# Optimization experiments

Measured on AMD Instinct MI355X. Metric: run time of the kernel, lower is better.

The kernel has to match this reference:

```python
import jax, jax.numpy as jnp
import numpy as np

ALPHA = 0.25
GAMMA = 2.0
COST_MASK = 1.0
COST_DICE = 1.0


def setup_inputs() -> dict:
    key = jax.random.key(0)
    k1, k2 = jax.random.split(key)
    B, N, M, H, W = 4, 100, 20, 256, 256
    outputs = jax.random.normal(k1, (B, N, H, W), dtype=jnp.float32)
    # binary target masks; threshold ensures every mask is non-empty so the
    # data-dependent tgt_ids truncation in the original is a no-op
    targets = (jax.random.uniform(k2, (B, M, H, W)) > 0.7).astype(jnp.float32)
    return {"outputs": outputs, "targets": targets}


def _cost_matrix(out_mask, tgt_mask):
    # out_mask: [N, HW] logits, tgt_mask: [M, HW] binary
    hw = out_mask.shape[1]
    prob = jax.nn.sigmoid(out_mask)
    # BCE-with-logits: target=1 -> softplus(-x); target=0 -> softplus(x)
    bce_pos = jax.nn.softplus(-out_mask)
    bce_neg = jax.nn.softplus(out_mask)
    focal_pos = ALPHA * (1.0 - prob) ** GAMMA * bce_pos            # [N, HW]
    focal_neg = (1.0 - ALPHA) * prob ** GAMMA * bce_neg            # [N, HW]
    cost_mask = (jnp.einsum('nc,mc->nm', focal_pos, tgt_mask)
                 + jnp.einsum('nc,mc->nm', focal_neg, 1.0 - tgt_mask)) / hw
    # dice cost
    numerator = 2.0 * jnp.einsum('nc,mc->nm', prob, tgt_mask)
    denominator = prob.sum(-1)[:, None] + tgt_mask.sum(-1)[None, :]
    cost_dice = 1.0 - (numerator + 1.0) / (denominator + 1.0)
    return COST_MASK * cost_mask + COST_DICE * cost_dice           # [N, M]


def reference(outputs, targets):
    B, N, H, W = outputs.shape
    M = targets.shape[1]
    out_flat = outputs.reshape(B, N, H * W)
    tgt_flat = targets.reshape(B, M, H * W)
    # vmap over batch: per-image [N, M] cost matrix fed to Hungarian on CPU
    C = jax.vmap(_cost_matrix)(out_flat, tgt_flat)  # [B, N, M]
    return C
```

## Files before the change

kernel.cpp:

```cpp
#include <hip/hip_runtime.h>

#define BB 4
#define NN 100
#define MM 20
#define HWPIX 65536
#define NT 7
#define GSEG 64
#define BLKPX (HWPIX / GSEG)
#define WAVEPX 256
#define NCHUNK (WAVEPX / 32)
#define PSLOTS 728

typedef float f32x4 __attribute__((ext_vector_type(4)));
typedef float f32x2 __attribute__((ext_vector_type(2)));
typedef short bf16x8 __attribute__((ext_vector_type(8)));
typedef unsigned int u32;
typedef unsigned int u32x4 __attribute__((ext_vector_type(4)));

static __device__ __forceinline__ u32 pkbf(float lo, float hi) {
    const u32 ul = __builtin_bit_cast(u32, lo) + 0x8000u;
    const u32 uh = __builtin_bit_cast(u32, hi) + 0x8000u;
    return __builtin_amdgcn_perm(uh, ul, 0x07060302u);
}

__global__ __launch_bounds__(256) void pack_kernel(
    const float* __restrict__ tgt,
    u32* __restrict__ masks)
{
    const int b = blockIdx.x >> 6;
    const int c = ((blockIdx.x & 63) << 10) | (threadIdx.x << 2);
    const float* tb = tgt + (size_t)b * MM * HWPIX + c;

    u32 mk0 = 0, mk1 = 0, mk2 = 0, mk3 = 0;
#pragma unroll
    for (int m = 0; m < MM; ++m) {
        const f32x4 t = *(const f32x4*)(tb + (size_t)m * HWPIX);
        mk0 |= (t.x > 0.5f) ? (1u << m) : 0u;
        mk1 |= (t.y > 0.5f) ? (1u << m) : 0u;
        mk2 |= (t.z > 0.5f) ? (1u << m) : 0u;
        mk3 |= (t.w > 0.5f) ? (1u << m) : 0u;
    }
    uint4 v; v.x = mk0; v.y = mk1; v.z = mk2; v.w = mk3;
    *(uint4*)(masks + (size_t)b * HWPIX + c) = v;
}

__global__ __launch_bounds__(256, 4) void cost_mfma_kernel(
    const float* __restrict__ out,
    const u32* __restrict__ masks,
    float* __restrict__ part)
{
    const int g    = blockIdx.x & (GSEG - 1);
    const int nt   = (blockIdx.x >> 6) % NT;
    const int b    = blockIdx.x / (GSEG * NT);
    const int tid  = threadIdx.x;
    const int w    = tid >> 6;
    const int lane = tid & 63;
    const int lrow = lane & 15;
    const int quad = lane >> 4;

    const int n = min(nt * 16 + lrow, NN - 1);
    const float* xrow = out + (size_t)(b * NN + n) * HWPIX;
    const u32*   mrow = masks + (size_t)b * HWPIX;

    const int kw = g * BLKPX + w * WAVEPX + quad * 8;

    f32x4 d1a = {0,0,0,0}, d1b = {0,0,0,0};
    f32x4 d2a = {0,0,0,0}, d2b = {0,0,0,0};
    f32x4 d3a = {0,0,0,0}, d3b = {0,0,0,0};
    f32x2 sfn2 = {0.f, 0.f}, sp2 = {0.f, 0.f};

    bf16x8 ones;
#pragma unroll
    for (int j = 0; j < 8; ++j) ones[j] = (short)0x3F80;

#define EVALPAIR(X0, X1, MK0, MK1, R)                                        \
    {                                                                        \
        const f32x2 x2  = {(X0), (X1)};                                      \
        const f32x2 xl  = x2 * 1.44269504f;                                  \
        const f32x2 ex  = {__builtin_amdgcn_exp2f(xl.x),                     \
                           __builtin_amdgcn_exp2f(xl.y)};                    \
        const f32x2 ope = ex + 1.f;                                          \
        const f32x2 lg  = {__builtin_amdgcn_logf(ope.x),                     \
                           __builtin_amdgcn_logf(ope.y)};                    \
        const f32x2 bn  = lg * 0.69314718f;                                  \
        const f32x2 bp  = bn - x2;                                           \
        const f32x2 rc  = {__builtin_amdgcn_rcpf(ope.x),                     \
                           __builtin_amdgcn_rcpf(ope.y)};                    \
        const f32x2 p   = ex * rc;                                           \
        const f32x2 om  = 1.f - p;                                           \
        const f32x2 a4  = om * 0.25f;                                        \
        const f32x2 fpv = a4 * om * bp;                                      \
        const f32x2 b4  = p * 0.75f;                                         \
        const f32x2 fnv = b4 * p * bn;                                       \
        const f32x2 df  = fpv - fnv;                                         \
        sfn2 += fnv; sp2 += p;                                               \
        fd_pk[R] = pkbf(df.x, df.y);                                         \
        fp_pk[R] = pkbf(p.x, p.y);                                           \
        const u32 us0 = (MK0) >> lrow, us1 = (MK1) >> lrow;                  \
        t0_pk[R] = ((us0 & 1u) * 0x3F80u) | (((us1 & 1u) * 0x3F80u) << 16);  \
        t1_pk[R] = (((us0 >> 16) & 1u) * 0x3F80u)                            \
                 | ((((us1 >> 16) & 1u) * 0x3F80u) << 16);                   \
    }

#pragma unroll
    for (int ch = 0; ch < NCHUNK; ++ch) {
        const int k0 = kw + ch * 32;
        const f32x4 xa = *(const f32x4*)(xrow + k0);
        const f32x4 xb = *(const f32x4*)(xrow + k0 + 4);
        const u32x4 qa = *(const u32x4*)(mrow + k0);
        const u32x4 qb = *(const u32x4*)(mrow + k0 + 4);

        u32x4 fd_pk, fp_pk, t0_pk, t1_pk;
        EVALPAIR(xa.x, xa.y, qa.x, qa.y, 0)
        EVALPAIR(xa.z, xa.w, qa.z, qa.w, 1)
        EVALPAIR(xb.x, xb.y, qb.x, qb.y, 2)
        EVALPAIR(xb.z, xb.w, qb.z, qb.w, 3)

        const bf16x8 fdv = __builtin_bit_cast(bf16x8, fd_pk);
        const bf16x8 fpr = __builtin_bit_cast(bf16x8, fp_pk);
        const bf16x8 t0  = __builtin_bit_cast(bf16x8, t0_pk);
        const bf16x8 t1  = __builtin_bit_cast(bf16x8, t1_pk);

        d1a = __builtin_amdgcn_mfma_f32_16x16x32_bf16(fdv,  t0, d1a, 0, 0, 0);
        d2a = __builtin_amdgcn_mfma_f32_16x16x32_bf16(fpr,  t0, d2a, 0, 0, 0);
        d3a = __builtin_amdgcn_mfma_f32_16x16x32_bf16(ones, t0, d3a, 0, 0, 0);
        d1b = __builtin_amdgcn_mfma_f32_16x16x32_bf16(fdv,  t1, d1b, 0, 0, 0);
        d2b = __builtin_amdgcn_mfma_f32_16x16x32_bf16(fpr,  t1, d2b, 0, 0, 0);
        d3b = __builtin_amdgcn_mfma_f32_16x16x32_bf16(ones, t1, d3b, 0, 0, 0);
    }
#undef EVALPAIR

    float sfn = sfn2.x + sfn2.y;
    float sp  = sp2.x + sp2.y;
    sfn += __shfl_xor(sfn, 16, 64); sfn += __shfl_xor(sfn, 32, 64);
    sp  += __shfl_xor(sp,  16, 64); sp  += __shfl_xor(sp,  32, 64);

    __shared__ float lds[4 * PSLOTS];
    float* lw = lds + w * PSLOTS;
#pragma unroll
    for (int r = 0; r < 4; ++r) {
        const int nl = quad * 4 + r;
        lw[nl * 44 + lrow]      = d1a[r];
        lw[nl * 44 + 20 + lrow] = d2a[r];
        if (lrow < 4) {
            lw[nl * 44 + 16 + lrow] = d1b[r];
            lw[nl * 44 + 36 + lrow] = d2b[r];
        }
    }
    if (lane < 16) {
        lw[lrow * 44 + 40] = sfn;
        lw[lrow * 44 + 41] = sp;
        lw[lrow * 44 + 42] = 0.f;
        lw[lrow * 44 + 43] = 0.f;
    }
    if (quad == 0) {
        lw[704 + lrow] = d3a[0];
        if (lrow < 4) lw[720 + lrow] = d3b[0];
    }
    if (quad == 1 && lrow < 4) lw[724 + lrow] = 0.f;
    __syncthreads();

    float* pout = part + (size_t)blockIdx.x * PSLOTS;
    for (int idx = tid; idx < PSLOTS; idx += 256)
        pout[idx] = lds[idx] + lds[PSLOTS + idx] + lds[2 * PSLOTS + idx]
                  + lds[3 * PSLOTS + idx];
}

__global__ __launch_bounds__(256) void combine_kernel(
    const float* __restrict__ part,
    float* __restrict__ C)
{
    const int bn = blockIdx.x;
    const int b  = bn / NN;
    const int n  = bn - b * NN;
    const int nt = n >> 4, nl = n & 15;
    const float* pbase = part + (size_t)((b * NT + nt) * GSEG) * PSLOTS;

    const int t  = threadIdx.x;
    const int s  = t & 63;
    const int gp = t >> 6;

    float acc = 0.f;
    if (s < 44) {
        const int off = nl * 44 + s;
#pragma unroll
        for (int gg = 0; gg < 16; ++gg)
            acc += pbase[(size_t)(gp * 16 + gg) * PSLOTS + off];
    } else {
        const int off = 704 + (s - 44);
#pragma unroll
        for (int gg = 0; gg < 16; ++gg)
            acc += pbase[(size_t)(gp * 16 + gg) * PSLOTS + off];
    }

    __shared__ float r1[4][64];
    r1[gp][s] = acc;
    __syncthreads();

    if (t < MM) {
        const int m = t;
        float D1 = 0.f, D2 = 0.f, SFN = 0.f, SP = 0.f, TS = 0.f;
#pragma unroll
        for (int g4 = 0; g4 < 4; ++g4) {
            D1  += r1[g4][m];
            D2  += r1[g4][20 + m];
            SFN += r1[g4][40];
            SP  += r1[g4][41];
            TS  += r1[g4][44 + m];
        }
        const float cost_mask = (SFN + D1) * (1.f / (float)HWPIX);
        const float den  = SP + TS;
        const float dice = 1.f - (2.f * D2 + 1.f) / (den + 1.f);
        C[bn * MM + m] = cost_mask + dice;
    }
}

extern "C" void kernel_launch(void* const* d_in, const int* in_sizes, int n_in,
                              void* d_out, int out_size, void* d_ws, size_t ws_size,
                              hipStream_t stream)
{
    const float* outp = (const float*)d_in[0];
    const float* tgtp = (const float*)d_in[1];
    float* C = (float*)d_out;

    char* ws = (char*)d_ws;
    u32* masks = (u32*)ws;
    float* part = (float*)(ws + (size_t)BB * HWPIX * sizeof(u32));

    pack_kernel<<<BB * 64, 256, 0, stream>>>(tgtp, masks);
    cost_mfma_kernel<<<BB * NT * GSEG, 256, 0, stream>>>(outp, masks, part);
    combine_kernel<<<BB * NN, 256, 0, stream>>>(part, C);
}
```

Measured before the change: 182.4 us.

## Stage logits through double-buffered LDS slabs with coalesced row loads

Global loads of the logits change from per-lane strided rows (16 rows × 8 pixels per quad) to fully coalesced 1KB row segments, one per wave-row. These are staged into a padded, double-buffered LDS tile, and each wave then reads its MFMA fragments from LDS. The next slab's global loads are issued before computing on the current one, to overlap memory and compute. The change adds LDS traffic and a __syncthreads per slab, and drops the occupancy hint in launch_bounds. The mask-bit to bf16 packing is also rewritten with selects instead of multiplies.

After: 179.8 us. About the same (-1.4%).

```diff
diff --git a/kernel.cpp b/kernel.cpp
--- a/kernel.cpp
+++ b/kernel.cpp
@@ -7,8 +7,9 @@
 #define NT 7
 #define GSEG 64
 #define BLKPX (HWPIX / GSEG)
-#define WAVEPX 256
-#define NCHUNK (WAVEPX / 32)
+#define SLABPX 256
+#define NSLAB (BLKPX / SLABPX)
+#define ROWSTR 260
 #define PSLOTS 728
 
 typedef float f32x4 __attribute__((ext_vector_type(4)));
@@ -44,7 +45,7 @@
     *(uint4*)(masks + (size_t)b * HWPIX + c) = v;
 }
 
-__global__ __launch_bounds__(256, 4) void cost_mfma_kernel(
+__global__ __launch_bounds__(256) void cost_mfma_kernel(
     const float* __restrict__ out,
     const u32* __restrict__ masks,
     float* __restrict__ part)
@@ -58,11 +59,15 @@
     const int lrow = lane & 15;
     const int quad = lane >> 4;
 
-    const int n = min(nt * 16 + lrow, NN - 1);
-    const float* xrow = out + (size_t)(b * NN + n) * HWPIX;
-    const u32*   mrow = masks + (size_t)b * HWPIX;
-
-    const int kw = g * BLKPX + w * WAVEPX + quad * 8;
+    __shared__ float ldsb[2 * 16 * ROWSTR];
+
+    const float* xrp[4];
+#pragma unroll
+    for (int r = 0; r < 4; ++r) {
+        const int n = min(nt * 16 + 4 * w + r, NN - 1);
+        xrp[r] = out + (size_t)(b * NN + n) * HWPIX + g * BLKPX + lane * 4;
+    }
+    const u32* mrow = masks + (size_t)b * HWPIX + g * BLKPX;
 
     f32x4 d1a = {0,0,0,0}, d1b = {0,0,0,0};
     f32x4 d2a = {0,0,0,0}, d2b = {0,0,0,0};
@@ -97,36 +102,63 @@
         fd_pk[R] = pkbf(df.x, df.y);                                         \
         fp_pk[R] = pkbf(p.x, p.y);                                           \
         const u32 us0 = (MK0) >> lrow, us1 = (MK1) >> lrow;                  \
-        t0_pk[R] = ((us0 & 1u) * 0x3F80u) | (((us1 & 1u) * 0x3F80u) << 16);  \
-        t1_pk[R] = (((us0 >> 16) & 1u) * 0x3F80u)                            \
-                 | ((((us1 >> 16) & 1u) * 0x3F80u) << 16);                   \
-    }
-
-#pragma unroll
-    for (int ch = 0; ch < NCHUNK; ++ch) {
-        const int k0 = kw + ch * 32;
-        const f32x4 xa = *(const f32x4*)(xrow + k0);
-        const f32x4 xb = *(const f32x4*)(xrow + k0 + 4);
-        const u32x4 qa = *(const u32x4*)(mrow + k0);
-        const u32x4 qb = *(const u32x4*)(mrow + k0 + 4);
-
-        u32x4 fd_pk, fp_pk, t0_pk, t1_pk;
-        EVALPAIR(xa.x, xa.y, qa.x, qa.y, 0)
-        EVALPAIR(xa.z, xa.w, qa.z, qa.w, 1)
-        EVALPAIR(xb.x, xb.y, qb.x, qb.y, 2)
-        EVALPAIR(xb.z, xb.w, qb.z, qb.w, 3)
-
-        const bf16x8 fdv = __builtin_bit_cast(bf16x8, fd_pk);
-        const bf16x8 fpr = __builtin_bit_cast(bf16x8, fp_pk);
-        const bf16x8 t0  = __builtin_bit_cast(bf16x8, t0_pk);
-        const bf16x8 t1  = __builtin_bit_cast(bf16x8, t1_pk);
-
-        d1a = __builtin_amdgcn_mfma_f32_16x16x32_bf16(fdv,  t0, d1a, 0, 0, 0);
-        d2a = __builtin_amdgcn_mfma_f32_16x16x32_bf16(fpr,  t0, d2a, 0, 0, 0);
-        d3a = __builtin_amdgcn_mfma_f32_16x16x32_bf16(ones, t0, d3a, 0, 0, 0);
-        d1b = __builtin_amdgcn_mfma_f32_16x16x32_bf16(fdv,  t1, d1b, 0, 0, 0);
-        d2b = __builtin_amdgcn_mfma_f32_16x16x32_bf16(fpr,  t1, d2b, 0, 0, 0);
-        d3b = __builtin_amdgcn_mfma_f32_16x16x32_bf16(ones, t1, d3b, 0, 0, 0);
+        t0_pk[R] = ((us0 & 1u) ? 0x3F80u : 0u)                               \
+                 | ((us1 & 1u) ? 0x3F800000u : 0u);                          \
+        t1_pk[R] = (((us0 >> 16) & 1u) ? 0x3F80u : 0u)                       \
+                 | (((us1 >> 16) & 1u) ? 0x3F800000u : 0u);                  \
+    }
+
+    f32x4 stage[4];
+#pragma unroll
+    for (int r = 0; r < 4; ++r) stage[r] = *(const f32x4*)(xrp[r]);
+#pragma unroll
+    for (int r = 0; r < 4; ++r)
+        *(f32x4*)&ldsb[(4 * w + r) * ROWSTR + lane * 4] = stage[r];
+    __syncthreads();
+
+    for (int s = 0; s < NSLAB; ++s) {
+        const int cur = s & 1, nxt = cur ^ 1;
+
+        if (s + 1 < NSLAB) {
+#pragma unroll
+            for (int r = 0; r < 4; ++r)
+                stage[r] = *(const f32x4*)(xrp[r] + (s + 1) * SLABPX);
+        }
+
+        const float* xl0 = &ldsb[cur * 16 * ROWSTR + lrow * ROWSTR + w * 64 + quad * 8];
+        const u32*   mp0 = mrow + s * SLABPX + w * 64 + quad * 8;
+#pragma unroll
+        for (int chl = 0; chl < 2; ++chl) {
+            const f32x4 xa = *(const f32x4*)(xl0 + chl * 32);
+            const f32x4 xb = *(const f32x4*)(xl0 + chl * 32 + 4);
+            const u32x4 qa = *(const u32x4*)(mp0 + chl * 32);
+            const u32x4 qb = *(const u32x4*)(mp0 + chl * 32 + 4);
+
+            u32x4 fd_pk, fp_pk, t0_pk, t1_pk;
+            EVALPAIR(xa.x, xa.y, qa.x, qa.y, 0)
+            EVALPAIR(xa.z, xa.w, qa.z, qa.w, 1)
+            EVALPAIR(xb.x, xb.y, qb.x, qb.y, 2)
+            EVALPAIR(xb.z, xb.w, qb.z, qb.w, 3)
+
+            const bf16x8 fdv = __builtin_bit_cast(bf16x8, fd_pk);
+            const bf16x8 fpr = __builtin_bit_cast(bf16x8, fp_pk);
+            const bf16x8 t0  = __builtin_bit_cast(bf16x8, t0_pk);
+            const bf16x8 t1  = __builtin_bit_cast(bf16x8, t1_pk);
+
+            d1a = __builtin_amdgcn_mfma_f32_16x16x32_bf16(fdv,  t0, d1a, 0, 0, 0);
+            d2a = __builtin_amdgcn_mfma_f32_16x16x32_bf16(fpr,  t0, d2a, 0, 0, 0);
+            d3a = __builtin_amdgcn_mfma_f32_16x16x32_bf16(ones, t0, d3a, 0, 0, 0);
+            d1b = __builtin_amdgcn_mfma_f32_16x16x32_bf16(fdv,  t1, d1b, 0, 0, 0);
+            d2b = __builtin_amdgcn_mfma_f32_16x16x32_bf16(fpr,  t1, d2b, 0, 0, 0);
+            d3b = __builtin_amdgcn_mfma_f32_16x16x32_bf16(ones, t1, d3b, 0, 0, 0);
+        }
+
+        if (s + 1 < NSLAB) {
+#pragma unroll
+            for (int r = 0; r < 4; ++r)
+                *(f32x4*)&ldsb[nxt * 16 * ROWSTR + (4 * w + r) * ROWSTR + lane * 4] = stage[r];
+        }
+        __syncthreads();
     }
 #undef EVALPAIR
 
@@ -135,8 +167,7 @@
     sfn += __shfl_xor(sfn, 16, 64); sfn += __shfl_xor(sfn, 32, 64);
     sp  += __shfl_xor(sp,  16, 64); sp  += __shfl_xor(sp,  32, 64);
 
-    __shared__ float lds[4 * PSLOTS];
-    float* lw = lds + w * PSLOTS;
+    float* lw = ldsb + w * PSLOTS;
 #pragma unroll
     for (int r = 0; r < 4; ++r) {
         const int nl = quad * 4 + r;
@@ -162,8 +193,8 @@
 
     float* pout = part + (size_t)blockIdx.x * PSLOTS;
     for (int idx = tid; idx < PSLOTS; idx += 256)
-        pout[idx] = lds[idx] + lds[PSLOTS + idx] + lds[2 * PSLOTS + idx]
-                  + lds[3 * PSLOTS + idx];
+        pout[idx] = ldsb[idx] + ldsb[PSLOTS + idx] + ldsb[2 * PSLOTS + idx]
+                  + ldsb[3 * PSLOTS + idx];
 }
 
 __global__ __launch_bounds__(256) void combine_kernel(
```

## Fold prob-sum and target-count into existing MFMAs, dropping ones-MFMAs

Applied to the files above, without the earlier changes.

The two extra MFMAs that multiplied a ones vector by the target masks are removed. Target pixel counts now come from a padded row (row 5 of the last n-tile, which is a clamped duplicate) whose prob operand is set to ones. The per-row prob sum comes from a spare target column (column 4 of the t1 operand) set to ones. This drops a third of the MFMA work and the scalar prob-sum accumulation, and shrinks the partial buffer. It also raises the occupancy hint to 6 blocks and limits loop unrolling to 2, which may trade register pressure against instruction-level parallelism.

After: 176.8 us. 3.0% less time.

```diff
diff --git a/kernel.cpp b/kernel.cpp
--- a/kernel.cpp
+++ b/kernel.cpp
@@ -9,7 +9,7 @@
 #define BLKPX (HWPIX / GSEG)
 #define WAVEPX 256
 #define NCHUNK (WAVEPX / 32)
-#define PSLOTS 728
+#define PSLOTS 704
 
 typedef float f32x4 __attribute__((ext_vector_type(4)));
 typedef float f32x2 __attribute__((ext_vector_type(2)));
@@ -44,7 +44,7 @@
     *(uint4*)(masks + (size_t)b * HWPIX + c) = v;
 }
 
-__global__ __launch_bounds__(256, 4) void cost_mfma_kernel(
+__global__ __launch_bounds__(256, 6) void cost_mfma_kernel(
     const float* __restrict__ out,
     const u32* __restrict__ masks,
     float* __restrict__ part)
@@ -58,6 +58,9 @@
     const int lrow = lane & 15;
     const int quad = lane >> 4;
 
+    const bool sp_col = (lrow == 4);
+    const bool ts_row = (nt == NT - 1) && (lrow == 5);
+
     const int n = min(nt * 16 + lrow, NN - 1);
     const float* xrow = out + (size_t)(b * NN + n) * HWPIX;
     const u32*   mrow = masks + (size_t)b * HWPIX;
@@ -66,12 +69,7 @@
 
     f32x4 d1a = {0,0,0,0}, d1b = {0,0,0,0};
     f32x4 d2a = {0,0,0,0}, d2b = {0,0,0,0};
-    f32x4 d3a = {0,0,0,0}, d3b = {0,0,0,0};
-    f32x2 sfn2 = {0.f, 0.f}, sp2 = {0.f, 0.f};
-
-    bf16x8 ones;
-#pragma unroll
-    for (int j = 0; j < 8; ++j) ones[j] = (short)0x3F80;
+    f32x2 sfn2 = {0.f, 0.f};
 
 #define EVALPAIR(X0, X1, MK0, MK1, R)                                        \
     {                                                                        \
@@ -93,16 +91,18 @@
         const f32x2 b4  = p * 0.75f;                                         \
         const f32x2 fnv = b4 * p * bn;                                       \
         const f32x2 df  = fpv - fnv;                                         \
-        sfn2 += fnv; sp2 += p;                                               \
+        sfn2 += fnv;                                                         \
         fd_pk[R] = pkbf(df.x, df.y);                                         \
-        fp_pk[R] = pkbf(p.x, p.y);                                           \
+        fp_pk[R] = ts_row ? 0x3F803F80u : pkbf(p.x, p.y);                    \
         const u32 us0 = (MK0) >> lrow, us1 = (MK1) >> lrow;                  \
-        t0_pk[R] = ((us0 & 1u) * 0x3F80u) | (((us1 & 1u) * 0x3F80u) << 16);  \
-        t1_pk[R] = (((us0 >> 16) & 1u) * 0x3F80u)                            \
-                 | ((((us1 >> 16) & 1u) * 0x3F80u) << 16);                   \
-    }
-
-#pragma unroll
+        t0_pk[R] = ((us0 & 1u) ? 0x3F80u : 0u)                               \
+                 | ((us1 & 1u) ? 0x3F800000u : 0u);                          \
+        const u32 t1c = (((us0 >> 16) & 1u) ? 0x3F80u : 0u)                  \
+                      | (((us1 >> 16) & 1u) ? 0x3F800000u : 0u);             \
+        t1_pk[R] = sp_col ? 0x3F803F80u : t1c;                               \
+    }
+
+#pragma unroll 2
     for (int ch = 0; ch < NCHUNK; ++ch) {
         const int k0 = kw + ch * 32;
         const f32x4 xa = *(const f32x4*)(xrow + k0);
@@ -121,19 +121,15 @@
         const bf16x8 t0  = __builtin_bit_cast(bf16x8, t0_pk);
         const bf16x8 t1  = __builtin_bit_cast(bf16x8, t1_pk);
 
-        d1a = __builtin_amdgcn_mfma_f32_16x16x32_bf16(fdv,  t0, d1a, 0, 0, 0);
-        d2a = __builtin_amdgcn_mfma_f32_16x16x32_bf16(fpr,  t0, d2a, 0, 0, 0);
-        d3a = __builtin_amdgcn_mfma_f32_16x16x32_bf16(ones, t0, d3a, 0, 0, 0);
-        d1b = __builtin_amdgcn_mfma_f32_16x16x32_bf16(fdv,  t1, d1b, 0, 0, 0);
-        d2b = __builtin_amdgcn_mfma_f32_16x16x32_bf16(fpr,  t1, d2b, 0, 0, 0);
-        d3b = __builtin_amdgcn_mfma_f32_16x16x32_bf16(ones, t1, d3b, 0, 0, 0);
+        d1a = __builtin_amdgcn_mfma_f32_16x16x32_bf16(fdv, t0, d1a, 0, 0, 0);
+        d2a = __builtin_amdgcn_mfma_f32_16x16x32_bf16(fpr, t0, d2a, 0, 0, 0);
+        d1b = __builtin_amdgcn_mfma_f32_16x16x32_bf16(fdv, t1, d1b, 0, 0, 0);
+        d2b = __builtin_amdgcn_mfma_f32_16x16x32_bf16(fpr, t1, d2b, 0, 0, 0);
     }
 #undef EVALPAIR
 
     float sfn = sfn2.x + sfn2.y;
-    float sp  = sp2.x + sp2.y;
     sfn += __shfl_xor(sfn, 16, 64); sfn += __shfl_xor(sfn, 32, 64);
-    sp  += __shfl_xor(sp,  16, 64); sp  += __shfl_xor(sp,  32, 64);
 
     __shared__ float lds[4 * PSLOTS];
     float* lw = lds + w * PSLOTS;
@@ -146,18 +142,13 @@
             lw[nl * 44 + 16 + lrow] = d1b[r];
             lw[nl * 44 + 36 + lrow] = d2b[r];
         }
+        if (lrow == 4) lw[nl * 44 + 41] = d2b[r];
     }
     if (lane < 16) {
         lw[lrow * 44 + 40] = sfn;
-        lw[lrow * 44 + 41] = sp;
         lw[lrow * 44 + 42] = 0.f;
         lw[lrow * 44 + 43] = 0.f;
     }
-    if (quad == 0) {
-        lw[704 + lrow] = d3a[0];
-        if (lrow < 4) lw[720 + lrow] = d3b[0];
-    }
-    if (quad == 1 && lrow < 4) lw[724 + lrow] = 0.f;
     __syncthreads();
 
     float* pout = part + (size_t)blockIdx.x * PSLOTS;
@@ -175,6 +166,7 @@
     const int n  = bn - b * NN;
     const int nt = n >> 4, nl = n & 15;
     const float* pbase = part + (size_t)((b * NT + nt) * GSEG) * PSLOTS;
+    const float* pts   = part + (size_t)((b * NT + (NT - 1)) * GSEG) * PSLOTS;
 
     const int t  = threadIdx.x;
     const int s  = t & 63;
@@ -187,10 +179,11 @@
         for (int gg = 0; gg < 16; ++gg)
             acc += pbase[(size_t)(gp * 16 + gg) * PSLOTS + off];
     } else {
-        const int off = 704 + (s - 44);
+        const int m   = s - 44;
+        const int off = 5 * 44 + (m < 16 ? 20 + m : 36 + (m - 16));
 #pragma unroll
         for (int gg = 0; gg < 16; ++gg)
-            acc += pbase[(size_t)(gp * 16 + gg) * PSLOTS + off];
+            acc += pts[(size_t)(gp * 16 + gg) * PSLOTS + off];
     }
 
     __shared__ float r1[4][64];
```
